# Kernel optimization log

Measured on AMD Instinct MI355X. Metric: run time of the kernel, lower is better.

## Reference

```python
import jax, jax.numpy as jnp
import numpy as np

B, S, D = 2, 1024, 4096
H, KVH = 32, 8
HD = D // H          # 128
N_REP = H // KVH     # 4
R = 2                # LoRA rank


def setup_inputs() -> dict:
    key = jax.random.key(0)
    ks = jax.random.split(key, 10)
    sc = 0.02
    x = jax.random.normal(ks[0], (B, S, D), jnp.float32)
    wq = jax.random.normal(ks[1], (D, H * HD), jnp.float32) * sc
    wk = jax.random.normal(ks[2], (D, KVH * HD), jnp.float32) * sc
    wv = jax.random.normal(ks[3], (D, KVH * HD), jnp.float32) * sc
    wo = jax.random.normal(ks[4], (H * HD, D), jnp.float32) * sc
    lora_q_a = jax.random.normal(ks[5], (D, R), jnp.float32) * sc
    lora_q_b = jax.random.normal(ks[6], (R, H * HD), jnp.float32) * sc
    lora_v_a = jax.random.normal(ks[7], (D, R), jnp.float32) * sc
    lora_v_b = jax.random.normal(ks[8], (R, KVH * HD), jnp.float32) * sc
    # RoPE frequencies: freqs_cis[t, i] = exp(1j * t * 10000^(-2i/HD))
    inv_freq = 1.0 / (10000.0 ** (jnp.arange(0, HD, 2, dtype=jnp.float32) / HD))  # [HD/2]
    t = jnp.arange(S, dtype=jnp.float32)
    ang = jnp.outer(t, inv_freq)                      # [S, HD/2]
    freqs_cos = jnp.cos(ang)
    freqs_sin = jnp.sin(ang)
    # causal additive mask [1, 1, S, S]
    mask = jnp.triu(jnp.full((S, S), -1e9, jnp.float32), k=1)[None, None]
    return {"x": x, "wq": wq, "wk": wk, "wv": wv, "wo": wo,
            "lora_q_a": lora_q_a, "lora_q_b": lora_q_b,
            "lora_v_a": lora_v_a, "lora_v_b": lora_v_b,
            "freqs_cos": freqs_cos, "freqs_sin": freqs_sin,
            "mask": mask, "start_pos": 0}


def _rope(t, cos, sin):
    # t: [B, S, h, HD]; pairs (even, odd) are (real, imag) of complex halves
    b, s, h, hd = t.shape
    tr = t.reshape(b, s, h, hd // 2, 2)
    a, bb = tr[..., 0], tr[..., 1]
    c = cos[None, :, None, :]
    sn = sin[None, :, None, :]
    out = jnp.stack([a * c - bb * sn, a * sn + bb * c], axis=-1)
    return out.reshape(b, s, h, hd)


def reference(x, wq, wk, wv, wo, lora_q_a, lora_q_b, lora_v_a, lora_v_b,
              freqs_cos, freqs_sin, mask, start_pos):
    # projections + LoRA (note: original Lora_layer applies NO scaling in forward)
    xq = x @ wq + (x @ lora_q_a) @ lora_q_b            # [B,S,H*HD]
    xk = x @ wk                                         # [B,S,KVH*HD]
    xv = x @ wv + (x @ lora_v_a) @ lora_v_b             # [B,S,KVH*HD]
    xq = xq.reshape(B, S, H, HD)
    xk = xk.reshape(B, S, KVH, HD)
    xv = xv.reshape(B, S, KVH, HD)
    xq = _rope(xq, freqs_cos, freqs_sin)
    xk = _rope(xk, freqs_cos, freqs_sin)
    # repeat_kv (GQA expansion): [B,S,KVH,HD] -> [B,S,H,HD]
    k = jnp.repeat(xk, N_REP, axis=2)
    v = jnp.repeat(xv, N_REP, axis=2)
    # attention
    scores = jnp.einsum('bshd,bthd->bhst', xq, k) / np.sqrt(HD).astype(np.float32)
    scores = scores + mask
    probs = jax.nn.softmax(scores.astype(jnp.float32), axis=-1).astype(xq.dtype)
    out = jnp.einsum('bhst,bthd->bshd', probs, v)       # [B,S,H,HD]
    out = out.reshape(B, S, H * HD) @ wo                # [B,S,D]
    return out
```

## Files before the change

kernel.cpp:

```cpp
#include <hip/hip_runtime.h>
#include <stdint.h>

#define B_ 2
#define S_ 1024
#define D_ 4096
#define H_ 32
#define KVH_ 8
#define HD_ 128

typedef short short8 __attribute__((ext_vector_type(8)));
typedef float floatx4 __attribute__((ext_vector_type(4)));

__device__ __forceinline__ ushort f2bf(float f) {
  union { float f; uint32_t u; } v; v.f = f;
  return (ushort)((v.u + 0x7FFFu + ((v.u >> 16) & 1u)) >> 16);
}
__device__ __forceinline__ float bf2f(ushort u) {
  union { uint32_t x; float f; } v; v.x = ((uint32_t)u) << 16; return v.f;
}

__device__ __forceinline__ void gload16(const void* g, void* l) {
  __builtin_amdgcn_global_load_lds((__attribute__((address_space(1))) void*)g,
                                   (__attribute__((address_space(3))) void*)l,
                                   16, 0, 0);
}

__global__ __launch_bounds__(256) void k_cvtlora(const float* __restrict__ x,
                                                 const float* __restrict__ qa,
                                                 const float* __restrict__ va,
                                                 ushort* __restrict__ xb,
                                                 float* __restrict__ xa) {
  const int row = blockIdx.x, t = threadIdx.x;
  const float* xr = x + (size_t)row * D_;
  ushort* xo = xb + (size_t)row * D_;
  float a0 = 0, a1 = 0, a2 = 0, a3 = 0;
#pragma unroll
  for (int it = 0; it < 4; it++) {
    const int i = it * 1024 + t * 4;
    float4 v = *(const float4*)(xr + i);
    ushort o4[4] = {f2bf(v.x), f2bf(v.y), f2bf(v.z), f2bf(v.w)};
    *(uint2*)(xo + i) = *(uint2*)o4;
    float4 q0 = *(const float4*)(qa + 2 * i);
    float4 q1 = *(const float4*)(qa + 2 * i + 4);
    float4 w0 = *(const float4*)(va + 2 * i);
    float4 w1 = *(const float4*)(va + 2 * i + 4);
    a0 += v.x * q0.x + v.y * q0.z + v.z * q1.x + v.w * q1.z;
    a1 += v.x * q0.y + v.y * q0.w + v.z * q1.y + v.w * q1.w;
    a2 += v.x * w0.x + v.y * w0.z + v.z * w1.x + v.w * w1.z;
    a3 += v.x * w0.y + v.y * w0.w + v.z * w1.y + v.w * w1.w;
  }
#pragma unroll
  for (int off = 32; off; off >>= 1) {
    a0 += __shfl_down(a0, off, 64);
    a1 += __shfl_down(a1, off, 64);
    a2 += __shfl_down(a2, off, 64);
    a3 += __shfl_down(a3, off, 64);
  }
  __shared__ float red[4][4];
  const int w = t >> 6, lane = t & 63;
  if (lane == 0) { red[w][0] = a0; red[w][1] = a1; red[w][2] = a2; red[w][3] = a3; }
  __syncthreads();
  if (t < 4)
    xa[(size_t)row * 4 + t] = red[0][t] + red[1][t] + red[2][t] + red[3][t];
}

__global__ __launch_bounds__(256) void k_trw2(const float* __restrict__ in0,
                                              const float* __restrict__ in1,
                                              ushort* __restrict__ out0,
                                              ushort* __restrict__ out1,
                                              int in_stride, int out_stride) {
  const float* in = blockIdx.z ? in1 : in0;
  ushort* out = blockIdx.z ? out1 : out0;
  __shared__ float t[64][65];
  const int n0 = blockIdx.x * 64, k0 = blockIdx.y * 64;
  const int c4 = (threadIdx.x & 15) * 4, r = threadIdx.x >> 4;
#pragma unroll
  for (int rr = 0; rr < 64; rr += 16) {
    float4 v = *(const float4*)&in[(size_t)(k0 + r + rr) * in_stride + n0 + c4];
    t[r + rr][c4] = v.x; t[r + rr][c4 + 1] = v.y;
    t[r + rr][c4 + 2] = v.z; t[r + rr][c4 + 3] = v.w;
  }
  __syncthreads();
#pragma unroll
  for (int rr = 0; rr < 64; rr += 16) {
    const int n = r + rr;
    ushort o4[4] = {f2bf(t[c4][n]), f2bf(t[c4 + 1][n]),
                    f2bf(t[c4 + 2][n]), f2bf(t[c4 + 3][n])};
    *(uint2*)&out[(size_t)(n0 + n) * out_stride + k0 + c4] = *(uint2*)o4;
  }
}

#define GBAR __builtin_amdgcn_s_barrier()
#define VMCNT0 asm volatile("s_waitcnt vmcnt(0)" ::: "memory")
#define VMCNT6 asm volatile("s_waitcnt vmcnt(6)" ::: "memory")

#define QSTG(T, SB) do {                                                     \
    const ushort* ga_ = A + (size_t)(m0 + w * 16 + qsr) * Kz + (T) * 64 + qsc; \
    char* la_ = qlds + (SB) * 65536 + w * 2048;                              \
    gload16(ga_, la_); gload16(ga_ + 8 * Kz, la_ + 1024);                    \
    _Pragma("unroll") for (int u_ = 0; u_ < 3; u_++) {                       \
      const ushort* gb_ = Bt + (size_t)(n0 + u_ * 128 + w * 16 + qsr) * Kz   \
                          + (T) * 64 + qsc;                                  \
      char* lb_ = qlds + (SB) * 65536 + 16384 + u_ * 16384 + w * 2048;       \
      gload16(gb_, lb_); gload16(gb_ + 8 * Kz, lb_ + 1024);                  \
    }                                                                        \
  } while (0)

__global__ __launch_bounds__(512, 2) void k_gemmq(const ushort* __restrict__ A,
                                                  const ushort* __restrict__ Bt,
                                                  ushort* __restrict__ Qb,
                                                  ushort* __restrict__ Kb,
                                                  ushort* __restrict__ Vt,
                                                  const float* __restrict__ xa,
                                                  const float* __restrict__ qb,
                                                  const float* __restrict__ vb,
                                                  const float* __restrict__ fcos,
                                                  const float* __restrict__ fsin) {
  __shared__ char qlds[131072];
  const int flat = blockIdx.y * 16 + blockIdx.x;
  const int swz_id = (flat & 7) * 32 + (flat >> 3);
  const int m0 = (swz_id >> 4) * 128, n0 = (swz_id & 15) * 384;
  const int tid = threadIdx.x, lane = tid & 63, w = tid >> 6;
  const int wr = w >> 2, wc = w & 3;
  const int lr = lane & 15, g = lane >> 4;
  const int swz = (lr & 7) * 16;
  const size_t Kz = 4096;
  const int qsr = lane >> 3;
  const int qsc = ((lane & 7) ^ (qsr & 7)) * 8;

  floatx4 acc[4][6] = {};
  short8 af[4][2], bfr[6][2];

  QSTG(0, 0);
  VMCNT0;
  GBAR;

  for (int t = 0; t < 64; ++t) {
    const int bu = t & 1;
    if (t + 1 < 64) QSTG(t + 1, bu ^ 1);
    const char* ab_ = qlds + bu * 65536 + (wr * 64 + lr) * 128;
#pragma unroll
    for (int fr = 0; fr < 4; fr++)
#pragma unroll
      for (int ks = 0; ks < 2; ks++)
        af[fr][ks] = *(const short8*)(ab_ + fr * 2048 + (((ks * 4 + g) * 16) ^ swz));
    const char* bb_ = qlds + bu * 65536 + 16384 + (wc * 32 + lr) * 128;
#pragma unroll
    for (int u = 0; u < 3; u++)
#pragma unroll
      for (int e = 0; e < 2; e++)
#pragma unroll
        for (int ks = 0; ks < 2; ks++)
          bfr[u * 2 + e][ks] = *(const short8*)(bb_ + u * 16384 + e * 2048 +
                                                (((ks * 4 + g) * 16) ^ swz));
    __builtin_amdgcn_s_setprio(1);
#pragma unroll
    for (int fr = 0; fr < 4; fr++)
#pragma unroll
      for (int u = 0; u < 6; u++)
#pragma unroll
        for (int ks = 0; ks < 2; ks++)
          acc[fr][u] = __builtin_amdgcn_mfma_f32_16x16x32_bf16(
              af[fr][ks], bfr[u][ks], acc[fr][u], 0, 0, 0);
    __builtin_amdgcn_s_setprio(0);
    VMCNT0;
    GBAR;
  }

#pragma unroll
  for (int fr = 0; fr < 4; fr++) {
    const int mb = m0 + wr * 64 + fr * 16 + g * 4;
    const int bb = mb >> 10, s0 = mb & 1023;
    float4 xa4[4];
#pragma unroll
    for (int r = 0; r < 4; r++) xa4[r] = *(const float4*)&xa[(size_t)(mb + r) * 4];
#pragma unroll
    for (int j = 0; j < 3; j++)
#pragma unroll
      for (int e = 0; e < 2; e++) {
        const int n = n0 + j * 128 + wc * 32 + e * 16 + lr;
        if (n < 5120) {
          const bool lq = (n < 4096);
          float b0 = 0.f, b1 = 0.f;
          if (lq) { b0 = qb[n]; b1 = qb[4096 + n]; }
          const int p = (n & 127) >> 1;
          const bool even = !(n & 1);
          const int d = n & 127;
          ushort* dst = lq ? (Qb + ((size_t)(bb * H_ + (n >> 7)) * S_) * HD_ + d)
                           : (Kb + ((size_t)(bb * KVH_ + ((n - 4096) >> 7)) * S_) * HD_ + d);
#pragma unroll
          for (int r = 0; r < 4; r++) {
            float cc = acc[fr][j * 2 + e][r];
            if (lq) cc += xa4[r].x * b0 + xa4[r].y * b1;
            float pv = __shfl_xor(cc, 1, 64);
            const int s = s0 + r;
            float c = fcos[s * 64 + p], sn = fsin[s * 64 + p];
            float o = even ? (cc * c - pv * sn) : (cc * c + pv * sn);
            dst[(size_t)s * HD_] = f2bf(o);
          }
        } else {
          const int vcol = n - 5120;
          const float b0 = vb[vcol], b1 = vb[1024 + vcol];
          ushort v4[4];
#pragma unroll
          for (int r = 0; r < 4; r++)
            v4[r] = f2bf(acc[fr][j * 2 + e][r] + xa4[r].z * b0 + xa4[r].w * b1);
          *(uint2*)&Vt[(size_t)((bb * 8 + (vcol >> 7)) * 128 + (vcol & 127)) * 1024 + s0] =
              *(uint2*)v4;
        }
      }
  }
}

#define OSTG(T, SB) do {                                                     \
    const ushort* ga_ = A + (size_t)(m0 + w * 16 + osr) * Kz + (T) * 64 + osc; \
    char* la_ = olds + (SB) * 49152 + w * 2048;                              \
    gload16(ga_, la_); gload16(ga_ + 8 * Kz, la_ + 1024);                    \
    _Pragma("unroll") for (int u_ = 0; u_ < 2; u_++) {                       \
      const ushort* gb_ = Bt + (size_t)(n0 + u_ * 128 + w * 16 + osr) * Kz + (T) * 64 + osc; \
      char* lb_ = olds + (SB) * 49152 + 16384 + u_ * 16384 + w * 2048;       \
      gload16(gb_, lb_); gload16(gb_ + 8 * Kz, lb_ + 1024);                  \
    }                                                                        \
  } while (0)

#define OTILE(T, RB) do {                                                    \
    if ((T) + 2 < 64) OSTG((T) + 2, ((RB) + 2) % 3);                         \
    const char* ab_ = olds + (RB) * 49152 + (wr * 64 + lr) * 128;            \
    _Pragma("unroll") for (int fr = 0; fr < 4; fr++)                         \
    _Pragma("unroll") for (int ks = 0; ks < 2; ks++)                         \
      af[fr][ks] = *(const short8*)(ab_ + fr * 2048 + (((ks * 4 + g) * 16) ^ swz)); \
    const char* bb_ = olds + (RB) * 49152 + 16384 + (wc * 32 + lr) * 128;    \
    _Pragma("unroll") for (int u_ = 0; u_ < 2; u_++)                         \
    _Pragma("unroll") for (int e_ = 0; e_ < 2; e_++)                         \
    _Pragma("unroll") for (int ks = 0; ks < 2; ks++)                         \
      bfr[u_ * 2 + e_][ks] = *(const short8*)(bb_ + u_ * 16384 + e_ * 2048 + (((ks * 4 + g) * 16) ^ swz)); \
    __builtin_amdgcn_s_setprio(1);                                           \
    _Pragma("unroll") for (int fr = 0; fr < 4; fr++)                         \
    _Pragma("unroll") for (int u_ = 0; u_ < 4; u_++)                         \
    _Pragma("unroll") for (int ks = 0; ks < 2; ks++)                         \
      acc[fr][u_] = __builtin_amdgcn_mfma_f32_16x16x32_bf16(                 \
          af[fr][ks], bfr[u_][ks], acc[fr][u_], 0, 0, 0);                    \
    __builtin_amdgcn_s_setprio(0);                                           \
    if ((T) + 2 < 64) { VMCNT6; } else { VMCNT0; }                           \
    GBAR;                                                                    \
  } while (0)

__global__ __launch_bounds__(512, 2) void k_gemmo(const ushort* __restrict__ A,
                                                  const ushort* __restrict__ Bt,
                                                  float* __restrict__ C) {
  __shared__ char olds[147456];
  const int flat = blockIdx.y * 16 + blockIdx.x;
  const int swz_id = (flat & 7) * 32 + (flat >> 3);
  const int m0 = (swz_id >> 4) * 128, n0 = (swz_id & 15) * 256;
  const int tid = threadIdx.x, lane = tid & 63, w = tid >> 6;
  const int wr = w >> 2, wc = w & 3;
  const int lr = lane & 15, g = lane >> 4;
  const int swz = (lr & 7) * 16;
  const size_t Kz = 4096;
  const int osr = lane >> 3;
  const int osc = ((lane & 7) ^ (osr & 7)) * 8;

  floatx4 acc[4][4] = {};
  short8 af[4][2], bfr[4][2];

  OSTG(0, 0); OSTG(1, 1);
  VMCNT6;
  GBAR;

  for (int tt = 0; tt < 63; tt += 3) {
    OTILE(tt + 0, 0);
    OTILE(tt + 1, 1);
    OTILE(tt + 2, 2);
  }
  OTILE(63, 0);

#pragma unroll
  for (int fr = 0; fr < 4; fr++) {
    const int mb = m0 + wr * 64 + fr * 16 + g * 4;
#pragma unroll
    for (int j = 0; j < 2; j++)
#pragma unroll
      for (int e = 0; e < 2; e++) {
        const int n = n0 + j * 128 + wc * 32 + e * 16 + lr;
#pragma unroll
        for (int r = 0; r < 4; r++)
          C[(size_t)(mb + r) * 4096 + n] = acc[fr][j * 2 + e][r];
      }
  }
}

#define FSTAGE(T, DB) do {                                                   \
    _Pragma("unroll") for (int i_ = 0; i_ < 4; i_++) {                       \
      gload16(Kg + (size_t)((T) * 64 + i_ * 16 + k_srow) * HD_ + k_scol,     \
              fls + (DB) * 16384 + i_ * 4096 + w * 1024);                    \
      gload16(Vg + (size_t)(i_ * 32 + v_srow) * S_ + (T) * 64 + v_scol,      \
              fls + 32768 + (DB) * 16384 + i_ * 4096 + w * 1024);            \
    }                                                                        \
  } while (0)

__global__ __launch_bounds__(256, 2) void k_flash(const ushort* __restrict__ Qb,
                                                  const ushort* __restrict__ Kb,
                                                  const ushort* __restrict__ Vt,
                                                  ushort* __restrict__ attn) {
  __shared__ char fls[81920];
  const int qblk = (gridDim.x - 1) - blockIdx.x;
  const int h = blockIdx.y, b = blockIdx.z;
  const int kvh = h >> 2;
  const int tid = threadIdx.x, w = tid >> 6, lane = tid & 63;
  const int lr = lane & 15, g = lane >> 4;
  const int swz = (lr & 7) * 16;
  const int qra = qblk * 128 + w * 16;
  const ushort* Qrow = Qb + ((size_t)(b * H_ + h) * S_ + qra + lr) * HD_;
  short8 qfa[4], qfb[4];
#pragma unroll
  for (int ks = 0; ks < 4; ks++) {
    qfa[ks] = *(const short8*)(Qrow + ks * 32 + g * 8);
    qfb[ks] = *(const short8*)(Qrow + 64 * HD_ + ks * 32 + g * 8);
  }
  const ushort* Kg = Kb + (size_t)(b * KVH_ + kvh) * S_ * HD_;
  const ushort* Vg = Vt + (size_t)(b * KVH_ + kvh) * HD_ * S_;
  char* Pw = fls + 65536 + w * 4096;
  const int q7 = lr & 7;
  const int k_srow = tid >> 4;
  const int k_scol = ((tid & 15) ^ (k_srow & 7)) * 8;
  const int v_srow = tid >> 3;
  const int v_scol = ((tid & 7) ^ (v_srow & 7)) * 8;
  const float scale = 0.088388347648318447f;

  float m_a = -1e30f, l_a = 0.f, m_b = -1e30f, l_b = 0.f;
  floatx4 oa[8] = {}, ob[8] = {};
  const int nt = 2 * qblk + 2;
  const int lastA = 2 * qblk;

  FSTAGE(0, 0);
  VMCNT0;
  GBAR;

  for (int t = 0; t < nt; t++) {
    const int cur = t & 1;
    if (t + 1 < nt) FSTAGE(t + 1, cur ^ 1);
    const char* Kl = fls + cur * 16384;
    const char* Vl = fls + 32768 + cur * 16384;
    if (t <= lastA) {
      floatx4 s4[4] = {};
      __builtin_amdgcn_s_setprio(1);
#pragma unroll
      for (int mf = 0; mf < 4; mf++) {
        const char* Krow = Kl + (mf * 16 + lr) * 256;
#pragma unroll
        for (int ks = 0; ks < 4; ks++) {
          short8 kf = *(const short8*)(Krow + (((ks * 4 + g) * 16) ^ swz));
          s4[mf] = __builtin_amdgcn_mfma_f32_16x16x32_bf16(kf, qfa[ks], s4[mf], 0, 0, 0);
        }
      }
      __builtin_amdgcn_s_setprio(0);
      float tm = -1e30f;
      if (t == lastA) {
#pragma unroll
        for (int mf = 0; mf < 4; mf++)
#pragma unroll
          for (int r = 0; r < 4; r++) {
            int kv = t * 64 + mf * 16 + g * 4 + r;
            float v = (kv > qra + lr) ? -1e30f : s4[mf][r] * scale;
            s4[mf][r] = v; tm = fmaxf(tm, v);
          }
      } else {
#pragma unroll
        for (int mf = 0; mf < 4; mf++)
#pragma unroll
          for (int r = 0; r < 4; r++) {
            float v = s4[mf][r] * scale;
            s4[mf][r] = v; tm = fmaxf(tm, v);
          }
      }
      tm = fmaxf(tm, __shfl_xor(tm, 16, 64));
      tm = fmaxf(tm, __shfl_xor(tm, 32, 64));
      float m_new = fmaxf(m_a, tm);
      float corr = __expf(m_a - m_new);
      float rs = 0.f;
#pragma unroll
      for (int mf = 0; mf < 4; mf++)
#pragma unroll
        for (int r = 0; r < 4; r++) {
          float p = __expf(s4[mf][r] - m_new);
          s4[mf][r] = p; rs += p;
        }
      rs += __shfl_xor(rs, 16, 64);
      rs += __shfl_xor(rs, 32, 64);
      l_a = l_a * corr + rs; m_a = m_new;
#pragma unroll
      for (int r = 0; r < 4; r++) {
        float cr = __shfl(corr, g * 4 + r, 64);
#pragma unroll
        for (int nf = 0; nf < 8; nf++) oa[nf][r] *= cr;
      }
#pragma unroll
      for (int mf = 0; mf < 4; mf++) {
        uint2 pv;
        pv.x = (uint32_t)f2bf(s4[mf][0]) | ((uint32_t)f2bf(s4[mf][1]) << 16);
        pv.y = (uint32_t)f2bf(s4[mf][2]) | ((uint32_t)f2bf(s4[mf][3]) << 16);
        *(uint2*)(Pw + lr * 128 + ((mf * 32 + g * 8) ^ (q7 << 4))) = pv;
      }
    }
    {
      floatx4 s4[4] = {};
      __builtin_amdgcn_s_setprio(1);
#pragma unroll
      for (int mf = 0; mf < 4; mf++) {
        const char* Krow = Kl + (mf * 16 + lr) * 256;
#pragma unroll
        for (int ks = 0; ks < 4; ks++) {
          short8 kf = *(const short8*)(Krow + (((ks * 4 + g) * 16) ^ swz));
          s4[mf] = __builtin_amdgcn_mfma_f32_16x16x32_bf16(kf, qfb[ks], s4[mf], 0, 0, 0);
        }
      }
      __builtin_amdgcn_s_setprio(0);
      float tm = -1e30f;
      if (t == nt - 1) {
#pragma unroll
        for (int mf = 0; mf < 4; mf++)
#pragma unroll
          for (int r = 0; r < 4; r++) {
            int kv = t * 64 + mf * 16 + g * 4 + r;
            float v = (kv > qra + 64 + lr) ? -1e30f : s4[mf][r] * scale;
            s4[mf][r] = v; tm = fmaxf(tm, v);
          }
      } else {
#pragma unroll
        for (int mf = 0; mf < 4; mf++)
#pragma unroll
          for (int r = 0; r < 4; r++) {
            float v = s4[mf][r] * scale;
            s4[mf][r] = v; tm = fmaxf(tm, v);
          }
      }
      tm = fmaxf(tm, __shfl_xor(tm, 16, 64));
      tm = fmaxf(tm, __shfl_xor(tm, 32, 64));
      float m_new = fmaxf(m_b, tm);
      float corr = __expf(m_b - m_new);
      float rs = 0.f;
#pragma unroll
      for (int mf = 0; mf < 4; mf++)
#pragma unroll
        for (int r = 0; r < 4; r++) {
          float p = __expf(s4[mf][r] - m_new);
          s4[mf][r] = p; rs += p;
        }
      rs += __shfl_xor(rs, 16, 64);
      rs += __shfl_xor(rs, 32, 64);
      l_b = l_b * corr + rs; m_b = m_new;
#pragma unroll
      for (int r = 0; r < 4; r++) {
        float cr = __shfl(corr, g * 4 + r, 64);
#pragma unroll
        for (int nf = 0; nf < 8; nf++) ob[nf][r] *= cr;
      }
#pragma unroll
      for (int mf = 0; mf < 4; mf++) {
        uint2 pv;
        pv.x = (uint32_t)f2bf(s4[mf][0]) | ((uint32_t)f2bf(s4[mf][1]) << 16);
        pv.y = (uint32_t)f2bf(s4[mf][2]) | ((uint32_t)f2bf(s4[mf][3]) << 16);
        *(uint2*)(Pw + 2048 + lr * 128 + ((mf * 32 + g * 8) ^ (q7 << 4))) = pv;
      }
    }
    __builtin_amdgcn_s_setprio(1);
#pragma unroll
    for (int ks2 = 0; ks2 < 2; ks2++) {
      short8 pb = *(const short8*)(Pw + 2048 + lr * 128 + ((ks2 * 64 + g * 16) ^ (q7 << 4)));
      short8 pa = pb;
      if (t <= lastA)
        pa = *(const short8*)(Pw + lr * 128 + ((ks2 * 64 + g * 16) ^ (q7 << 4)));
#pragma unroll
      for (int nf = 0; nf < 8; nf++) {
        short8 vf = *(const short8*)(Vl + (nf * 16 + lr) * 128 + (((ks2 * 4 + g) * 16) ^ swz));
        if (t <= lastA)
          oa[nf] = __builtin_amdgcn_mfma_f32_16x16x32_bf16(pa, vf, oa[nf], 0, 0, 0);
        ob[nf] = __builtin_amdgcn_mfma_f32_16x16x32_bf16(pb, vf, ob[nf], 0, 0, 0);
      }
    }
    __builtin_amdgcn_s_setprio(0);
    VMCNT0;
    GBAR;
  }
  const float linva = 1.0f / l_a, linvb = 1.0f / l_b;
  ushort* outp = attn + ((size_t)(b * S_) + qra) * 4096 + h * 128;
#pragma unroll
  for (int r = 0; r < 4; r++) {
    float lia = __shfl(linva, g * 4 + r, 64);
    float lib = __shfl(linvb, g * 4 + r, 64);
    ushort* orow = outp + (size_t)(g * 4 + r) * 4096;
#pragma unroll
    for (int nf = 0; nf < 8; nf++) {
      orow[nf * 16 + lr] = f2bf(oa[nf][r] * lia);
      orow[(size_t)64 * 4096 + nf * 16 + lr] = f2bf(ob[nf][r] * lib);
    }
  }
}

extern "C" void kernel_launch(void* const* d_in, const int* in_sizes, int n_in,
                              void* d_out, int out_size, void* d_ws, size_t ws_size,
                              hipStream_t stream) {
  (void)in_sizes; (void)n_in; (void)out_size; (void)ws_size;
  const float* x    = (const float*)d_in[0];
  const float* wq   = (const float*)d_in[1];
  const float* wk   = (const float*)d_in[2];
  const float* wv   = (const float*)d_in[3];
  const float* wo   = (const float*)d_in[4];
  const float* lqa  = (const float*)d_in[5];
  const float* lqb  = (const float*)d_in[6];
  const float* lva  = (const float*)d_in[7];
  const float* lvb  = (const float*)d_in[8];
  const float* fcos = (const float*)d_in[9];
  const float* fsin = (const float*)d_in[10];

  char* ws = (char*)d_ws;
  ushort* xb   = (ushort*)(ws + 0);
  ushort* wT   = (ushort*)(ws + 16777216);
  ushort* woT  = (ushort*)(ws + 67108864);
  ushort* Qb   = (ushort*)(ws + 150994944);
  ushort* Kb   = (ushort*)(ws + 167772160);
  ushort* Vt   = (ushort*)(ws + 171966464);
  ushort* attn = (ushort*)(ws + 176160768);
  float*  xa   = (float*) (ws + 192937984);

  k_cvtlora<<<2048, 256, 0, stream>>>(x, lqa, lva, xb, xa);
  k_trw2<<<dim3(64, 64, 2), 256, 0, stream>>>(wq, wo, wT, woT, 4096, 4096);
  k_trw2<<<dim3(16, 64, 2), 256, 0, stream>>>(wk, wv, wT + (size_t)4096 * 4096,
                                              wT + (size_t)5120 * 4096, 1024, 4096);
  k_gemmq<<<dim3(16, 16), 512, 0, stream>>>(xb, wT, Qb, Kb, Vt, xa, lqb, lvb,
                                            fcos, fsin);
  k_flash<<<dim3(8, 32, 2), 256, 0, stream>>>(Qb, Kb, Vt, attn);
  k_gemmo<<<dim3(16, 16), 512, 0, stream>>>(attn, woT, (float*)d_out);
}
```

Before: 291.5 us.

## Double flash-attention query tile to 256 rows with 8 waves per block

The flash kernel now processes 256 query rows per block with 512 threads (8 waves), so each K/V tile staged in LDS serves twice as many queries. Causal limits are tracked per wave with separate last-tile bounds for the two row halves, and the async load staging is reindexed for the larger thread count. The grid halves to 256 blocks and LDS use grows to 96KB, which can lower occupancy and worsen load balance across the causal triangle. Waves whose rows are already done still wait at every block barrier.

```diff
diff --git a/kernel.cpp b/kernel.cpp
--- a/kernel.cpp
+++ b/kernel.cpp
@@ -290,47 +290,50 @@
 }
 
 #define FSTAGE(T, DB) do {                                                   \
-    _Pragma("unroll") for (int i_ = 0; i_ < 4; i_++) {                       \
-      gload16(Kg + (size_t)((T) * 64 + i_ * 16 + k_srow) * HD_ + k_scol,     \
-              fls + (DB) * 16384 + i_ * 4096 + w * 1024);                    \
-      gload16(Vg + (size_t)(i_ * 32 + v_srow) * S_ + (T) * 64 + v_scol,      \
-              fls + 32768 + (DB) * 16384 + i_ * 4096 + w * 1024);            \
-    }                                                                        \
+    gload16(Kg + (size_t)((T) * 64 + krow) * HD_ + kcol,                     \
+            fls + (DB) * 16384 + w * 1024);                                  \
+    gload16(Kg + (size_t)((T) * 64 + 32 + krow) * HD_ + kcol,                \
+            fls + (DB) * 16384 + 8192 + w * 1024);                           \
+    gload16(Vg + (size_t)vrow * S_ + (T) * 64 + vcol,                        \
+            fls + 32768 + (DB) * 16384 + w * 1024);                          \
+    gload16(Vg + (size_t)(64 + vrow) * S_ + (T) * 64 + vcol,                 \
+            fls + 32768 + (DB) * 16384 + 8192 + w * 1024);                   \
   } while (0)
 
-__global__ __launch_bounds__(256, 2) void k_flash(const ushort* __restrict__ Qb,
+__global__ __launch_bounds__(512, 2) void k_flash(const ushort* __restrict__ Qb,
                                                   const ushort* __restrict__ Kb,
                                                   const ushort* __restrict__ Vt,
                                                   ushort* __restrict__ attn) {
-  __shared__ char fls[81920];
-  const int qblk = (gridDim.x - 1) - blockIdx.x;
+  __shared__ char fls[98304];
+  const int qblk = 3 - blockIdx.x;
   const int h = blockIdx.y, b = blockIdx.z;
   const int kvh = h >> 2;
   const int tid = threadIdx.x, w = tid >> 6, lane = tid & 63;
   const int lr = lane & 15, g = lane >> 4;
   const int swz = (lr & 7) * 16;
-  const int qra = qblk * 128 + w * 16;
+  const int qra = qblk * 256 + w * 16;
   const ushort* Qrow = Qb + ((size_t)(b * H_ + h) * S_ + qra + lr) * HD_;
   short8 qfa[4], qfb[4];
 #pragma unroll
   for (int ks = 0; ks < 4; ks++) {
     qfa[ks] = *(const short8*)(Qrow + ks * 32 + g * 8);
-    qfb[ks] = *(const short8*)(Qrow + 64 * HD_ + ks * 32 + g * 8);
+    qfb[ks] = *(const short8*)(Qrow + 128 * HD_ + ks * 32 + g * 8);
   }
   const ushort* Kg = Kb + (size_t)(b * KVH_ + kvh) * S_ * HD_;
   const ushort* Vg = Vt + (size_t)(b * KVH_ + kvh) * HD_ * S_;
   char* Pw = fls + 65536 + w * 4096;
   const int q7 = lr & 7;
-  const int k_srow = tid >> 4;
-  const int k_scol = ((tid & 15) ^ (k_srow & 7)) * 8;
-  const int v_srow = tid >> 3;
-  const int v_scol = ((tid & 7) ^ (v_srow & 7)) * 8;
+  const int krow = tid >> 4;
+  const int kcol = ((tid & 15) ^ (krow & 7)) * 8;
+  const int vrow = tid >> 3;
+  const int vcol = ((tid & 7) ^ (vrow & 7)) * 8;
   const float scale = 0.088388347648318447f;
 
   float m_a = -1e30f, l_a = 0.f, m_b = -1e30f, l_b = 0.f;
   floatx4 oa[8] = {}, ob[8] = {};
-  const int nt = 2 * qblk + 2;
-  const int lastA = 2 * qblk;
+  const int nt = 4 * qblk + 4;
+  const int lastA = 4 * qblk + (w >> 2);
+  const int lastB = lastA + 2;
 
   FSTAGE(0, 0);
   VMCNT0;
@@ -402,7 +405,7 @@
         *(uint2*)(Pw + lr * 128 + ((mf * 32 + g * 8) ^ (q7 << 4))) = pv;
       }
     }
-    {
+    if (t <= lastB) {
       floatx4 s4[4] = {};
       __builtin_amdgcn_s_setprio(1);
 #pragma unroll
@@ -416,13 +419,13 @@
       }
       __builtin_amdgcn_s_setprio(0);
       float tm = -1e30f;
-      if (t == nt - 1) {
+      if (t == lastB) {
 #pragma unroll
         for (int mf = 0; mf < 4; mf++)
 #pragma unroll
           for (int r = 0; r < 4; r++) {
             int kv = t * 64 + mf * 16 + g * 4 + r;
-            float v = (kv > qra + 64 + lr) ? -1e30f : s4[mf][r] * scale;
+            float v = (kv > qra + 128 + lr) ? -1e30f : s4[mf][r] * scale;
             s4[mf][r] = v; tm = fmaxf(tm, v);
           }
       } else {
@@ -466,16 +469,18 @@
     __builtin_amdgcn_s_setprio(1);
 #pragma unroll
     for (int ks2 = 0; ks2 < 2; ks2++) {
-      short8 pb = *(const short8*)(Pw + 2048 + lr * 128 + ((ks2 * 64 + g * 16) ^ (q7 << 4)));
-      short8 pa = pb;
+      short8 pa, pb;
       if (t <= lastA)
         pa = *(const short8*)(Pw + lr * 128 + ((ks2 * 64 + g * 16) ^ (q7 << 4)));
+      if (t <= lastB)
+        pb = *(const short8*)(Pw + 2048 + lr * 128 + ((ks2 * 64 + g * 16) ^ (q7 << 4)));
 #pragma unroll
       for (int nf = 0; nf < 8; nf++) {
         short8 vf = *(const short8*)(Vl + (nf * 16 + lr) * 128 + (((ks2 * 4 + g) * 16) ^ swz));
         if (t <= lastA)
           oa[nf] = __builtin_amdgcn_mfma_f32_16x16x32_bf16(pa, vf, oa[nf], 0, 0, 0);
-        ob[nf] = __builtin_amdgcn_mfma_f32_16x16x32_bf16(pb, vf, ob[nf], 0, 0, 0);
+        if (t <= lastB)
+          ob[nf] = __builtin_amdgcn_mfma_f32_16x16x32_bf16(pb, vf, ob[nf], 0, 0, 0);
       }
     }
     __builtin_amdgcn_s_setprio(0);
@@ -492,7 +497,7 @@
 #pragma unroll
     for (int nf = 0; nf < 8; nf++) {
       orow[nf * 16 + lr] = f2bf(oa[nf][r] * lia);
-      orow[(size_t)64 * 4096 + nf * 16 + lr] = f2bf(ob[nf][r] * lib);
+      orow[(size_t)128 * 4096 + nf * 16 + lr] = f2bf(ob[nf][r] * lib);
     }
   }
 }
@@ -529,6 +534,6 @@
                                               wT + (size_t)5120 * 4096, 1024, 4096);
   k_gemmq<<<dim3(16, 16), 512, 0, stream>>>(xb, wT, Qb, Kb, Vt, xa, lqb, lvb,
                                             fcos, fsin);
-  k_flash<<<dim3(8, 32, 2), 256, 0, stream>>>(Qb, Kb, Vt, attn);
+  k_flash<<<dim3(4, 32, 2), 512, 0, stream>>>(Qb, Kb, Vt, attn);
   k_gemmo<<<dim3(16, 16), 512, 0, stream>>>(attn, woT, (float*)d_out);
 }
```

After: 293.9 us. No clear change (+0.8%).
